# Kernel tuning notes

Measured on AMD Instinct MI355X. Metric: run time of the kernel, lower is better.

## Reference

```python
import jax, jax.numpy as jnp
import numpy as np

B = 2048
D = 256
C = 100000
SCALE = 30.0
MARGIN = 0.2
EPS = 1e-6


def setup_inputs() -> dict:
    key = jax.random.key(0)
    k1, k2, k3 = jax.random.split(key, 3)
    emb = jax.random.normal(k1, (B, D), dtype=jnp.float32)
    # speaker embeddings are typically L2-normalized; also keeps cosines in (-1,1)
    emb = emb / jnp.linalg.norm(emb, axis=1, keepdims=True)
    W = jax.random.normal(k2, (C, D), dtype=jnp.float32)
    targets = jax.random.randint(k3, (B,), 0, C, dtype=jnp.int64)
    return {"embedding": emb, "W": W, "targets": targets}


def reference(embedding, W, targets):
    # normalize classifier rows (F.normalize on weight, dim=1, eps=1e-12)
    Wn = W / jnp.maximum(jnp.linalg.norm(W, axis=1, keepdims=True), 1e-12)
    # [B, C] cosine logits, clamped as in the original
    cos = jnp.clip(embedding @ Wn.T, -1.0, 1.0)
    # per-sample target cosine -> margin-adjusted numerator
    tgt_cos = jnp.take_along_axis(cos, targets[:, None], axis=1)[:, 0]
    numerator = SCALE * jnp.cos(jnp.arccos(tgt_cos) + MARGIN)  # [B]
    # masked sum over non-target classes (replaces the python loop + cat)
    col = jnp.arange(C, dtype=targets.dtype)[None, :]
    not_target = (col != targets[:, None]).astype(cos.dtype)  # [B, C]
    excl_sum = jnp.sum(jnp.exp(SCALE * cos) * not_target, axis=1)  # [B]
    denominator = jnp.exp(numerator) + excl_sum
    loss = -jnp.mean(numerator - jnp.log(denominator + EPS))
    return loss
```

## Files before the change

### kernel.cpp

```cpp
#include <hip/hip_runtime.h>
#include <hip/hip_bf16.h>


static constexpr int Bn = 2048;
static constexpr int Dn = 256;
static constexpr int Cn = 100000;
static constexpr int NSLICE = 1564;
static constexpr int CPAD   = NSLICE * 64;
static constexpr float OOB_COLS = (float)(CPAD - Cn);
static constexpr int NT = Bn / 16;

#define SCALE_F 30.0f
#define MARGIN_F 0.2f
#define EPS_F 1e-6f

typedef __attribute__((ext_vector_type(8))) short bf16x8;
typedef __attribute__((ext_vector_type(4))) float f32x4;

__device__ __forceinline__ short f2bf_rne(float x) {
    union { float f; unsigned int u; } v; v.f = x;
    unsigned int r = v.u + 0x7fffu + ((v.u >> 16) & 1u);
    return (short)(r >> 16);
}

__global__ __launch_bounds__(256) void k_prep(const float* __restrict__ W,
                                              const float* __restrict__ emb,
                                              const int* __restrict__ tgt,
                                              short* __restrict__ embF,
                                              float* __restrict__ numv,
                                              float* __restrict__ etv) {
    const int blk = blockIdx.x;
    if (blk < 256) {
        const int t     = blk >> 1;
        const int chunk = (blk & 1) * 256 + threadIdx.x;
        const int ks    = chunk >> 6;
        const int lane  = chunk & 63;
        const int q     = lane >> 4;
        const int cr    = lane & 15;
        const float* src = emb + (size_t)(t * 16 + cr) * Dn + ks * 32 + q * 8;
        float4 x0 = *(const float4*)(src);
        float4 x1 = *(const float4*)(src + 4);
        bf16x8 o;
        o[0] = f2bf_rne(x0.x); o[1] = f2bf_rne(x0.y);
        o[2] = f2bf_rne(x0.z); o[3] = f2bf_rne(x0.w);
        o[4] = f2bf_rne(x1.x); o[5] = f2bf_rne(x1.y);
        o[6] = f2bf_rne(x1.z); o[7] = f2bf_rne(x1.w);
        *(bf16x8*)(embF + (size_t)((t * 8 + ks) * 64 + lane) * 8) = o;
    } else {
        const int b    = (blk - 256) * 4 + (threadIdx.x >> 6);
        const int lane = threadIdx.x & 63;
        const int t    = tgt[b];
        float4 x = *(const float4*)(W + (size_t)t * Dn + lane * 4);
        float4 e = *(const float4*)(emb + b * Dn + lane * 4);
        float dot = x.x * e.x + x.y * e.y + x.z * e.z + x.w * e.w;
        float ss  = x.x * x.x + x.y * x.y + x.z * x.z + x.w * x.w;
#pragma unroll
        for (int o = 1; o < 64; o <<= 1) {
            dot += __shfl_xor(dot, o);
            ss  += __shfl_xor(ss, o);
        }
        if (lane == 0) {
            float cosv = dot / fmaxf(sqrtf(ss), 1e-12f);
            cosv = fminf(fmaxf(cosv, -1.f), 1.f);
            const float num = SCALE_F * cosf(acosf(cosv) + MARGIN_F);
            numv[b] = num;
            etv[b]  = __expf(SCALE_F * cosv);
        }
    }
}

__global__ __launch_bounds__(64, 2) void k_main(const float* __restrict__ W,
                                                const short* __restrict__ embF,
                                                float* __restrict__ partial) {
    const int lane = threadIdx.x;
    const int q    = lane >> 4;
    const int cr   = lane & 15;
    const int sl   = blockIdx.x;
    const int cbase = sl * 64;

    bf16x8 afrag[4][8];
#pragma unroll
    for (int ct = 0; ct < 4; ++ct) {
        const int c = cbase + ct * 16 + cr;
        const float* wr = W + (size_t)c * Dn;
        float ss = 0.0f;
        if (c < Cn) {
#pragma unroll
            for (int ks = 0; ks < 8; ++ks) {
                float4 x0 = *(const float4*)(wr + ks * 32 + q * 8);
                float4 x1 = *(const float4*)(wr + ks * 32 + q * 8 + 4);
                ss += x0.x * x0.x + x0.y * x0.y + x0.z * x0.z + x0.w * x0.w;
                ss += x1.x * x1.x + x1.y * x1.y + x1.z * x1.z + x1.w * x1.w;
            }
        }
        ss += __shfl_xor(ss, 16);
        ss += __shfl_xor(ss, 32);
        const float rn = 1.0f / fmaxf(sqrtf(ss), 1e-12f);
#pragma unroll
        for (int ks = 0; ks < 8; ++ks) {
            bf16x8 a = {0, 0, 0, 0, 0, 0, 0, 0};
            if (c < Cn) {
                float4 x0 = *(const float4*)(wr + ks * 32 + q * 8);
                float4 x1 = *(const float4*)(wr + ks * 32 + q * 8 + 4);
                a[0] = f2bf_rne(x0.x * rn); a[1] = f2bf_rne(x0.y * rn);
                a[2] = f2bf_rne(x0.z * rn); a[3] = f2bf_rne(x0.w * rn);
                a[4] = f2bf_rne(x1.x * rn); a[5] = f2bf_rne(x1.y * rn);
                a[6] = f2bf_rne(x1.z * rn); a[7] = f2bf_rne(x1.w * rn);
            }
            afrag[ct][ks] = a;
        }
    }

    float* pout = partial + (size_t)sl * Bn;
    const bf16x8* bsrc = (const bf16x8*)embF;

    auto load_b = [&](bf16x8* bf, int t) {
        const bf16x8* p = bsrc + (size_t)t * 512 + lane;
#pragma unroll
        for (int ks = 0; ks < 8; ++ks) bf[ks] = p[ks * 64];
    };

    auto compute = [&](const bf16x8* bf, int t) {
        f32x4 a0 = {0.f, 0.f, 0.f, 0.f};
        f32x4 a1 = {0.f, 0.f, 0.f, 0.f};
        f32x4 a2 = {0.f, 0.f, 0.f, 0.f};
        f32x4 a3 = {0.f, 0.f, 0.f, 0.f};
#pragma unroll
        for (int ks = 0; ks < 8; ++ks) {
            a0 = __builtin_amdgcn_mfma_f32_16x16x32_bf16(afrag[0][ks], bf[ks], a0, 0, 0, 0);
            a1 = __builtin_amdgcn_mfma_f32_16x16x32_bf16(afrag[1][ks], bf[ks], a1, 0, 0, 0);
            a2 = __builtin_amdgcn_mfma_f32_16x16x32_bf16(afrag[2][ks], bf[ks], a2, 0, 0, 0);
            a3 = __builtin_amdgcn_mfma_f32_16x16x32_bf16(afrag[3][ks], bf[ks], a3, 0, 0, 0);
        }
        float s = 0.0f;
#pragma unroll
        for (int r = 0; r < 4; ++r) {
            s += __expf(SCALE_F * a0[r]);
            s += __expf(SCALE_F * a1[r]);
            s += __expf(SCALE_F * a2[r]);
            s += __expf(SCALE_F * a3[r]);
        }
        s += __shfl_xor(s, 16);
        s += __shfl_xor(s, 32);
        if (lane < 16) pout[t * 16 + cr] = s;
    };

    bf16x8 b0[8], b1[8];
    load_b(b0, 0);
    for (int t = 0; t < NT; t += 2) {
        load_b(b1, t + 1);
        compute(b0, t);
        load_b(b0, (t + 2) < NT ? (t + 2) : 0);
        compute(b1, t + 1);
    }
}

__global__ __launch_bounds__(256) void k_finish(const float* __restrict__ partial,
                                                const float* __restrict__ numv,
                                                const float* __restrict__ etv,
                                                float* __restrict__ out) {
    __shared__ float red[64];
    const int l  = threadIdx.x & 63;
    const int qq = threadIdx.x >> 6;
    const int b  = blockIdx.x * 64 + l;

    if (threadIdx.x < 64) red[threadIdx.x] = 0.0f;
    __syncthreads();

    const int s0 = qq * (NSLICE / 4);
    const int s1 = s0 + (NSLICE / 4);
    float acc = 0.0f;
    for (int s = s0; s < s1; ++s) acc += partial[(size_t)s * Bn + b];
    atomicAdd(&red[l], acc);
    __syncthreads();

    if (threadIdx.x < 64) {
        const float num  = numv[b];
        const float excl = red[l] - OOB_COLS - etv[b];
        const float denom = __expf(num) + excl;
        float term = num - logf(denom + EPS_F);
#pragma unroll
        for (int o = 1; o < 64; o <<= 1) term += __shfl_xor(term, o);
        if (l == 0) atomicAdd(out, -term / (float)Bn);
    }
}

extern "C" void kernel_launch(void* const* d_in, const int* in_sizes, int n_in,
                              void* d_out, int out_size, void* d_ws, size_t ws_size,
                              hipStream_t stream) {
    const float* emb = (const float*)d_in[0];
    const float* W   = (const float*)d_in[1];
    const int*   tgt = (const int*)d_in[2];
    float* out = (float*)d_out;

    char* ws = (char*)d_ws;
    short* embF    = (short*)ws;
    float* partial = (float*)(ws + (1 << 20));
    float* numv    = partial + (size_t)NSLICE * Bn;
    float* etv     = numv + Bn;

    hipMemsetAsync(out, 0, sizeof(float), stream);
    k_prep<<<768, 256, 0, stream>>>(W, emb, tgt, embF, numv, etv);
    k_main<<<NSLICE, 64, 0, stream>>>(W, embF, partial);
    k_finish<<<32, 256, 0, stream>>>(partial, numv, etv, out);
}
```

Before: 272.1 us.

## Split batch across 4x more waves, atomic-accumulate sums, fold scale into exp2

Each 64-class slice is now split into four batch quarters, so the main kernel launches four times as many single-wave blocks, with a block-index remap that spreads work across XCDs. Per-row exp sums are accumulated with global atomics into a B-length buffer instead of a [NSLICE, B] partial array, which shrinks the finish kernel to a trivial pass. SCALE*log2(e) is folded into the bf16 embedding so the inner loop uses raw exp2 with split accumulators. In exchange, each W slice's normalization and bf16 conversion is repeated four times, there is heavy atomic traffic on 2048 addresses, and the larger pre-scaled bf16 values lose some relative precision.

```diff
diff --git a/kernel.cpp b/kernel.cpp
--- a/kernel.cpp
+++ b/kernel.cpp
@@ -6,13 +6,16 @@
 static constexpr int Dn = 256;
 static constexpr int Cn = 100000;
 static constexpr int NSLICE = 1564;
+static constexpr int SSPLIT = 4;
 static constexpr int CPAD   = NSLICE * 64;
 static constexpr float OOB_COLS = (float)(CPAD - Cn);
-static constexpr int NT = Bn / 16;
+static constexpr int NT  = Bn / 16;
+static constexpr int NTW = NT / SSPLIT;
 
 #define SCALE_F 30.0f
 #define MARGIN_F 0.2f
 #define EPS_F 1e-6f
+#define L2E_SCALE 43.2808512266689f
 
 typedef __attribute__((ext_vector_type(8))) short bf16x8;
 typedef __attribute__((ext_vector_type(4))) float f32x4;
@@ -41,10 +44,10 @@
         float4 x0 = *(const float4*)(src);
         float4 x1 = *(const float4*)(src + 4);
         bf16x8 o;
-        o[0] = f2bf_rne(x0.x); o[1] = f2bf_rne(x0.y);
-        o[2] = f2bf_rne(x0.z); o[3] = f2bf_rne(x0.w);
-        o[4] = f2bf_rne(x1.x); o[5] = f2bf_rne(x1.y);
-        o[6] = f2bf_rne(x1.z); o[7] = f2bf_rne(x1.w);
+        o[0] = f2bf_rne(x0.x * L2E_SCALE); o[1] = f2bf_rne(x0.y * L2E_SCALE);
+        o[2] = f2bf_rne(x0.z * L2E_SCALE); o[3] = f2bf_rne(x0.w * L2E_SCALE);
+        o[4] = f2bf_rne(x1.x * L2E_SCALE); o[5] = f2bf_rne(x1.y * L2E_SCALE);
+        o[6] = f2bf_rne(x1.z * L2E_SCALE); o[7] = f2bf_rne(x1.w * L2E_SCALE);
         *(bf16x8*)(embF + (size_t)((t * 8 + ks) * 64 + lane) * 8) = o;
     } else {
         const int b    = (blk - 256) * 4 + (threadIdx.x >> 6);
@@ -71,12 +74,17 @@
 
 __global__ __launch_bounds__(64, 2) void k_main(const float* __restrict__ W,
                                                 const short* __restrict__ embF,
-                                                float* __restrict__ partial) {
+                                                float* __restrict__ acc) {
     const int lane = threadIdx.x;
     const int q    = lane >> 4;
     const int cr   = lane & 15;
-    const int sl   = blockIdx.x;
+
+    const int grp = (NSLICE * SSPLIT) >> 3;
+    const int w   = (blockIdx.x & 7) * grp + (blockIdx.x >> 3);
+    const int sl  = w >> 2;
+    const int h   = w & 3;
     const int cbase = sl * 64;
+    const int t0    = h * NTW;
 
     bf16x8 afrag[4][8];
 #pragma unroll
@@ -111,7 +119,6 @@
         }
     }
 
-    float* pout = partial + (size_t)sl * Bn;
     const bf16x8* bsrc = (const bf16x8*)embF;
 
     auto load_b = [&](bf16x8* bf, int t) {
@@ -132,57 +139,41 @@
             a2 = __builtin_amdgcn_mfma_f32_16x16x32_bf16(afrag[2][ks], bf[ks], a2, 0, 0, 0);
             a3 = __builtin_amdgcn_mfma_f32_16x16x32_bf16(afrag[3][ks], bf[ks], a3, 0, 0, 0);
         }
-        float s = 0.0f;
+        float s0 = 0.f, s1 = 0.f, s2 = 0.f, s3 = 0.f;
 #pragma unroll
         for (int r = 0; r < 4; ++r) {
-            s += __expf(SCALE_F * a0[r]);
-            s += __expf(SCALE_F * a1[r]);
-            s += __expf(SCALE_F * a2[r]);
-            s += __expf(SCALE_F * a3[r]);
+            s0 += __builtin_amdgcn_exp2f(a0[r]);
+            s1 += __builtin_amdgcn_exp2f(a1[r]);
+            s2 += __builtin_amdgcn_exp2f(a2[r]);
+            s3 += __builtin_amdgcn_exp2f(a3[r]);
         }
+        float s = (s0 + s1) + (s2 + s3);
         s += __shfl_xor(s, 16);
         s += __shfl_xor(s, 32);
-        if (lane < 16) pout[t * 16 + cr] = s;
+        if (lane < 16) atomicAdd(&acc[t * 16 + cr], s);
     };
 
     bf16x8 b0[8], b1[8];
-    load_b(b0, 0);
-    for (int t = 0; t < NT; t += 2) {
-        load_b(b1, t + 1);
-        compute(b0, t);
-        load_b(b0, (t + 2) < NT ? (t + 2) : 0);
-        compute(b1, t + 1);
+    load_b(b0, t0);
+    for (int i = 0; i < NTW; i += 2) {
+        load_b(b1, t0 + i + 1);
+        compute(b0, t0 + i);
+        load_b(b0, (i + 2) < NTW ? (t0 + i + 2) : t0);
+        compute(b1, t0 + i + 1);
     }
 }
 
-__global__ __launch_bounds__(256) void k_finish(const float* __restrict__ partial,
-                                                const float* __restrict__ numv,
-                                                const float* __restrict__ etv,
-                                                float* __restrict__ out) {
-    __shared__ float red[64];
-    const int l  = threadIdx.x & 63;
-    const int qq = threadIdx.x >> 6;
-    const int b  = blockIdx.x * 64 + l;
-
-    if (threadIdx.x < 64) red[threadIdx.x] = 0.0f;
-    __syncthreads();
-
-    const int s0 = qq * (NSLICE / 4);
-    const int s1 = s0 + (NSLICE / 4);
-    float acc = 0.0f;
-    for (int s = s0; s < s1; ++s) acc += partial[(size_t)s * Bn + b];
-    atomicAdd(&red[l], acc);
-    __syncthreads();
-
-    if (threadIdx.x < 64) {
-        const float num  = numv[b];
-        const float excl = red[l] - OOB_COLS - etv[b];
-        const float denom = __expf(num) + excl;
-        float term = num - logf(denom + EPS_F);
+__global__ __launch_bounds__(64) void k_finish(const float* __restrict__ acc,
+                                               const float* __restrict__ numv,
+                                               const float* __restrict__ etv,
+                                               float* __restrict__ out) {
+    const int b = blockIdx.x * 64 + threadIdx.x;
+    const float num  = numv[b];
+    const float excl = acc[b] - OOB_COLS - etv[b];
+    float term = num - logf(__expf(num) + excl + EPS_F);
 #pragma unroll
-        for (int o = 1; o < 64; o <<= 1) term += __shfl_xor(term, o);
-        if (l == 0) atomicAdd(out, -term / (float)Bn);
-    }
+    for (int o = 1; o < 64; o <<= 1) term += __shfl_xor(term, o);
+    if (threadIdx.x == 0) atomicAdd(out, -term / (float)Bn);
 }
 
 extern "C" void kernel_launch(void* const* d_in, const int* in_sizes, int n_in,
@@ -194,13 +185,14 @@
     float* out = (float*)d_out;
 
     char* ws = (char*)d_ws;
-    short* embF    = (short*)ws;
-    float* partial = (float*)(ws + (1 << 20));
-    float* numv    = partial + (size_t)NSLICE * Bn;
-    float* etv     = numv + Bn;
+    short* embF = (short*)ws;
+    float* acc  = (float*)(ws + (1 << 20));
+    float* numv = acc + Bn;
+    float* etv  = numv + Bn;
 
     hipMemsetAsync(out, 0, sizeof(float), stream);
+    hipMemsetAsync(acc, 0, Bn * sizeof(float), stream);
     k_prep<<<768, 256, 0, stream>>>(W, emb, tgt, embF, numv, etv);
-    k_main<<<NSLICE, 64, 0, stream>>>(W, embF, partial);
-    k_finish<<<32, 256, 0, stream>>>(partial, numv, etv, out);
+    k_main<<<NSLICE * SSPLIT, 64, 0, stream>>>(W, embF, acc);
+    k_finish<<<Bn / 64, 64, 0, stream>>>(acc, numv, etv, out);
 }
```

After: 352.5 us. +29.5%, slower.

## Split batch tiles across four waves sharing LDS-staged class fragments; fold scale into exp2

Applied to the files above, without the earlier changes.

Each block of k_main now runs four wavefronts instead of one. Each wave normalizes and converts one 16-class tile of W into shared memory, then every wave reads all four A fragments back and handles a quarter of the batch tiles. This spreads the serial W-prep and the 128-tile MFMA loop across four waves, which should raise parallelism and latency hiding. The constant SCALE*log2(e) is folded into the bf16 embedding in k_prep so the inner loop can use raw exp2 with split accumulators. The cost is extra rounding from the scaled bf16 values and higher register and LDS pressure per block.

```diff
diff --git a/kernel.cpp b/kernel.cpp
--- a/kernel.cpp
+++ b/kernel.cpp
@@ -8,11 +8,14 @@
 static constexpr int NSLICE = 1564;
 static constexpr int CPAD   = NSLICE * 64;
 static constexpr float OOB_COLS = (float)(CPAD - Cn);
-static constexpr int NT = Bn / 16;
+static constexpr int NT  = Bn / 16;
+static constexpr int NWV = 4;
+static constexpr int NTW = NT / NWV;
 
 #define SCALE_F 30.0f
 #define MARGIN_F 0.2f
 #define EPS_F 1e-6f
+#define L2E_SCALE 43.2808512266689f
 
 typedef __attribute__((ext_vector_type(8))) short bf16x8;
 typedef __attribute__((ext_vector_type(4))) float f32x4;
@@ -41,10 +44,10 @@
         float4 x0 = *(const float4*)(src);
         float4 x1 = *(const float4*)(src + 4);
         bf16x8 o;
-        o[0] = f2bf_rne(x0.x); o[1] = f2bf_rne(x0.y);
-        o[2] = f2bf_rne(x0.z); o[3] = f2bf_rne(x0.w);
-        o[4] = f2bf_rne(x1.x); o[5] = f2bf_rne(x1.y);
-        o[6] = f2bf_rne(x1.z); o[7] = f2bf_rne(x1.w);
+        o[0] = f2bf_rne(x0.x * L2E_SCALE); o[1] = f2bf_rne(x0.y * L2E_SCALE);
+        o[2] = f2bf_rne(x0.z * L2E_SCALE); o[3] = f2bf_rne(x0.w * L2E_SCALE);
+        o[4] = f2bf_rne(x1.x * L2E_SCALE); o[5] = f2bf_rne(x1.y * L2E_SCALE);
+        o[6] = f2bf_rne(x1.z * L2E_SCALE); o[7] = f2bf_rne(x1.w * L2E_SCALE);
         *(bf16x8*)(embF + (size_t)((t * 8 + ks) * 64 + lane) * 8) = o;
     } else {
         const int b    = (blk - 256) * 4 + (threadIdx.x >> 6);
@@ -69,19 +72,20 @@
     }
 }
 
-__global__ __launch_bounds__(64, 2) void k_main(const float* __restrict__ W,
-                                                const short* __restrict__ embF,
-                                                float* __restrict__ partial) {
-    const int lane = threadIdx.x;
+__global__ __launch_bounds__(256, 2) void k_main(const float* __restrict__ W,
+                                                 const short* __restrict__ embF,
+                                                 float* __restrict__ partial) {
+    __shared__ short afrag_sh[4 * 8 * 64 * 8];
+    const int tid  = threadIdx.x;
+    const int lane = tid & 63;
+    const int wv   = tid >> 6;
     const int q    = lane >> 4;
     const int cr   = lane & 15;
     const int sl   = blockIdx.x;
     const int cbase = sl * 64;
 
-    bf16x8 afrag[4][8];
-#pragma unroll
-    for (int ct = 0; ct < 4; ++ct) {
-        const int c = cbase + ct * 16 + cr;
+    {
+        const int c = cbase + wv * 16 + cr;
         const float* wr = W + (size_t)c * Dn;
         float ss = 0.0f;
         if (c < Cn) {
@@ -107,12 +111,21 @@
                 a[4] = f2bf_rne(x1.x * rn); a[5] = f2bf_rne(x1.y * rn);
                 a[6] = f2bf_rne(x1.z * rn); a[7] = f2bf_rne(x1.w * rn);
             }
-            afrag[ct][ks] = a;
-        }
-    }
+            *(bf16x8*)(afrag_sh + (size_t)((wv * 8 + ks) * 64 + lane) * 8) = a;
+        }
+    }
+    __syncthreads();
+
+    bf16x8 afrag[4][8];
+#pragma unroll
+    for (int ct = 0; ct < 4; ++ct)
+#pragma unroll
+        for (int ks = 0; ks < 8; ++ks)
+            afrag[ct][ks] = *(const bf16x8*)(afrag_sh + (size_t)((ct * 8 + ks) * 64 + lane) * 8);
 
     float* pout = partial + (size_t)sl * Bn;
     const bf16x8* bsrc = (const bf16x8*)embF;
+    const int t0 = wv * NTW;
 
     auto load_b = [&](bf16x8* bf, int t) {
         const bf16x8* p = bsrc + (size_t)t * 512 + lane;
@@ -132,26 +145,27 @@
             a2 = __builtin_amdgcn_mfma_f32_16x16x32_bf16(afrag[2][ks], bf[ks], a2, 0, 0, 0);
             a3 = __builtin_amdgcn_mfma_f32_16x16x32_bf16(afrag[3][ks], bf[ks], a3, 0, 0, 0);
         }
-        float s = 0.0f;
+        float s0 = 0.f, s1 = 0.f, s2 = 0.f, s3 = 0.f;
 #pragma unroll
         for (int r = 0; r < 4; ++r) {
-            s += __expf(SCALE_F * a0[r]);
-            s += __expf(SCALE_F * a1[r]);
-            s += __expf(SCALE_F * a2[r]);
-            s += __expf(SCALE_F * a3[r]);
-        }
+            s0 += __builtin_amdgcn_exp2f(a0[r]);
+            s1 += __builtin_amdgcn_exp2f(a1[r]);
+            s2 += __builtin_amdgcn_exp2f(a2[r]);
+            s3 += __builtin_amdgcn_exp2f(a3[r]);
+        }
+        float s = (s0 + s1) + (s2 + s3);
         s += __shfl_xor(s, 16);
         s += __shfl_xor(s, 32);
         if (lane < 16) pout[t * 16 + cr] = s;
     };
 
     bf16x8 b0[8], b1[8];
-    load_b(b0, 0);
-    for (int t = 0; t < NT; t += 2) {
-        load_b(b1, t + 1);
-        compute(b0, t);
-        load_b(b0, (t + 2) < NT ? (t + 2) : 0);
-        compute(b1, t + 1);
+    load_b(b0, t0);
+    for (int i = 0; i < NTW; i += 2) {
+        load_b(b1, t0 + i + 1);
+        compute(b0, t0 + i);
+        load_b(b0, (i + 2) < NTW ? (t0 + i + 2) : t0);
+        compute(b1, t0 + i + 1);
     }
 }
 
@@ -201,6 +215,6 @@
 
     hipMemsetAsync(out, 0, sizeof(float), stream);
     k_prep<<<768, 256, 0, stream>>>(W, emb, tgt, embF, numv, etv);
-    k_main<<<NSLICE, 64, 0, stream>>>(W, embF, partial);
+    k_main<<<NSLICE, 256, 0, stream>>>(W, embF, partial);
     k_finish<<<32, 256, 0, stream>>>(partial, numv, etv, out);
 }
```

New measurement: 258.8 us. -4.9%, faster.
